# Kernel optimization log

Hardware: AMD Instinct MI355X
Metric: run time of the kernel (lower is better)

Reference implementation:

```python
import jax, jax.numpy as jnp
import numpy as np

H = 4          # attention_heads
TOPK = 101     # hard-coded [:101] in ContextModule.forward
EPS = 1e-5     # nn.LayerNorm default eps


def _linear(x, w, b):
    # torch nn.Linear: y = x @ W^T + b
    return x @ w.T + b


def _layer_norm(x, g, b):
    mu = jnp.mean(x, axis=-1, keepdims=True)
    var = jnp.var(x, axis=-1, keepdims=True)
    return (x - mu) * jax.lax.rsqrt(var + EPS) * g + b


def setup_inputs() -> dict:
    key = jax.random.key(0)
    ks = jax.random.split(key, 12)
    D, N, B, T = 512, 2000, 8, 1024
    s = 0.02
    f32 = jnp.float32
    return {
        "context_emb": jax.random.normal(ks[0], (N, D), f32),
        "encoder_out": jax.random.normal(ks[1], (B, T, D), f32),
        "wq": jax.random.normal(ks[2], (D, D), f32) * s,
        "bq": jnp.zeros((D,), f32),
        "wk": jax.random.normal(ks[3], (D, D), f32) * s,
        "bk": jnp.zeros((D,), f32),
        "wv": jax.random.normal(ks[4], (D, D), f32) * s,
        "bv": jnp.zeros((D,), f32),
        "wo": jax.random.normal(ks[5], (D, D), f32) * s,
        "bo": jnp.zeros((D,), f32),
        "w_comb": jax.random.normal(ks[6], (D, D), f32) * s,
        "b_comb": jnp.zeros((D,), f32),
        "ln_g": jnp.ones((D,), f32),
        "ln_b": jnp.zeros((D,), f32),
    }


def reference(context_emb, encoder_out, wq, bq, wk, bk, wv, bv, wo, bo,
              w_comb, b_comb, ln_g, ln_b):
    biasing_score = 1.0
    B, T, D = encoder_out.shape
    dk = D // H
    scale = 1.0 / np.sqrt(dk).astype(np.float32)

    # expand context to batch: [B, N, D]
    ctx = jnp.broadcast_to(context_emb, (B,) + context_emb.shape)

    # --- pass 1: attention matrix for scoring (get_attn_mat) ---
    q = _linear(encoder_out, wq, bq).reshape(B, T, H, dk).transpose(0, 2, 1, 3)  # bhtd
    k = _linear(ctx, wk, bk).reshape(B, -1, H, dk).transpose(0, 2, 1, 3)         # bhnd
    scores = jnp.einsum('bhtd,bhnd->bhtn', q, k) * scale
    attn = jax.nn.softmax(scores, axis=-1)                                        # [B,H,T,N]

    # attn_mat[0].sum(0).sum(0): per-context-phrase aggregate score -> [N]
    context_scores = attn[0].sum(axis=(0, 1))
    # torch.sort(descending)[1][:101] == top-101 indices by score
    _, idx = jax.lax.top_k(context_scores, TOPK)

    # gather filtered context embeddings: [B, 101, D]
    ctx_f = ctx[:, idx, :]

    # --- pass 2: full MHA on filtered context ---
    k2 = _linear(ctx_f, wk, bk).reshape(B, TOPK, H, dk).transpose(0, 2, 1, 3)
    v2 = _linear(ctx_f, wv, bv).reshape(B, TOPK, H, dk).transpose(0, 2, 1, 3)
    a2 = jax.nn.softmax(jnp.einsum('bhtd,bhnd->bhtn', q, k2) * scale, axis=-1)
    o = jnp.einsum('bhtn,bhnd->bhtd', a2, v2).transpose(0, 2, 1, 3).reshape(B, T, D)
    o = _linear(o, wo, bo)

    # combiner + residual + LayerNorm
    out = encoder_out + _linear(o, w_comb, b_comb) * biasing_score
    return _layer_norm(out, ln_g, ln_b)
```

## Files before the change

### kernel.cpp

```cpp
#include <hip/hip_runtime.h>
#include <hip/hip_bf16.h>


typedef short bhalf8 __attribute__((ext_vector_type(8)));
typedef float f32x4 __attribute__((ext_vector_type(4)));

#define SCALE 0.08838834764831845f

#define OFF_QBF    ((size_t)0)
#define OFF_RB     ((size_t)6193152)
#define OFF_TMP    ((size_t)8290304)
#define OFF_PART   (OFF_TMP)
#define OFF_CS     (OFF_TMP + 1024000)
#define OFF_IDX    (OFF_TMP + 1026048)
#define OFF_RSP    (OFF_TMP + 1026176)
#define OFF_CEBF   ((size_t)12484608)
#define OFF_K2BF   ((size_t)13022608)
#define OFF_V2TP   ((size_t)13074608)
#define OFF_WQBF   ((size_t)13107376)
#define OFF_WKBF   ((size_t)13238448)
#define OFF_WVBF   ((size_t)13369520)
#define OFF_WCBF   ((size_t)13500592)
#define OFF_WOTBF  ((size_t)13631664)
#define OFF_WC2BF  ((size_t)13762736)
#define OFF_BC2    ((size_t)13893808)

__device__ __forceinline__ float bf2f(short u) {
    union { float f; unsigned int i; } x;
    x.i = ((unsigned int)(unsigned short)u) << 16;
    return x.f;
}
__device__ __forceinline__ ushort f2b(float f) {
    union { float f; unsigned int i; } x; x.f = f;
    return (ushort)((x.i + 0x7fff + ((x.i >> 16) & 1)) >> 16);
}

__device__ __forceinline__ void gld16(ushort* lds, const ushort* g) {
    __builtin_amdgcn_global_load_lds(
        (const __attribute__((address_space(1))) unsigned int*)g,
        (__attribute__((address_space(3))) unsigned int*)lds, 16, 0, 0);
}

__global__ __launch_bounds__(256) void prep_kernel(
    const float* __restrict__ enc, const float* __restrict__ ce,
    const float* __restrict__ wq, const float* __restrict__ wk,
    const float* __restrict__ wv, const float* __restrict__ wc,
    const float* __restrict__ wo, const float* __restrict__ bo,
    const float* __restrict__ bcb,
    ushort* __restrict__ encbf, ushort* __restrict__ cebf,
    ushort* __restrict__ wqbf, ushort* __restrict__ wkbf,
    ushort* __restrict__ wvbf, ushort* __restrict__ wcbf,
    ushort* __restrict__ v2tp, ushort* __restrict__ wotbf,
    float* __restrict__ bc2)
{
    __shared__ float tile[32][33];
    const int b = blockIdx.x, tid = threadIdx.x;
    const float* s; ushort* d; int n4, base;
    if (b < 4096)      { s = enc; d = encbf; n4 = 1048576; base = b; }
    else if (b < 5096) { s = ce;  d = cebf;  n4 = 256000;  base = b - 4096; }
    else if (b < 5352) { s = wq;  d = wqbf;  n4 = 65536;   base = b - 5096; }
    else if (b < 5608) { s = wk;  d = wkbf;  n4 = 65536;   base = b - 5352; }
    else if (b < 5864) { s = wv;  d = wvbf;  n4 = 65536;   base = b - 5608; }
    else if (b < 6120) { s = wc;  d = wcbf;  n4 = 65536;   base = b - 5864; }
    else if (b < 6152) {
        const int i = (b - 6120) * 256 + tid;
        ((uint4*)v2tp)[i] = make_uint4(0u, 0u, 0u, 0u);
        return;
    } else if (b < 6154) {
        const int dd = (b - 6152) * 256 + tid;
        float acc = bcb[dd];
        const float4* wr = (const float4*)(wc + (size_t)dd * 512);
        const float4* br = (const float4*)bo;
        for (int m4 = 0; m4 < 128; ++m4) {
            const float4 w4 = wr[m4], b4 = br[m4];
            acc += w4.x * b4.x + w4.y * b4.y + w4.z * b4.z + w4.w * b4.w;
        }
        bc2[dd] = acc;
        return;
    } else {
        const int b2 = b - 6154;
        const int bx = (b2 & 15) * 32, by = (b2 >> 4) * 32;
        const int tx = tid & 31, ty = tid >> 5;
        #pragma unroll
        for (int rr = 0; rr < 4; ++rr)
            tile[ty + 8 * rr][tx] = wo[(size_t)(by + ty + 8 * rr) * 512 + bx + tx];
        __syncthreads();
        #pragma unroll
        for (int rr = 0; rr < 4; ++rr)
            wotbf[(size_t)(bx + ty + 8 * rr) * 512 + by + tx] =
                f2b(tile[tx][ty + 8 * rr]);
        return;
    }
    const int i = base * 256 + tid;
    if (i >= n4) return;
    const float4 v = ((const float4*)s)[i];
    ushort4 r;
    r.x = f2b(v.x); r.y = f2b(v.y); r.z = f2b(v.z); r.w = f2b(v.w);
    ((ushort4*)d)[i] = r;
}

__device__ __forceinline__ void gemm_body_512(
    const ushort* A, const ushort* W, const float* bias, ushort* Cbf,
    int M, int bm, int bn, ushort* As, ushort* Bs)
{
    const int tid = threadIdx.x;
    const int wave = tid >> 6, lane = tid & 63;
    const int wm = wave >> 1, wn = wave & 1;
    const int mr = lane & 15, g = lane >> 4;

    f32x4 acc[2][4];
    #pragma unroll
    for (int i = 0; i < 2; ++i)
        #pragma unroll
        for (int j = 0; j < 4; ++j)
            #pragma unroll
            for (int p = 0; p < 4; ++p) acc[i][j][p] = 0.f;

    const int r0 = tid >> 2, c0 = tid & 3;
    const int cA = (c0 ^ (r0 & 3)) * 8;
    const int rA  = min(bm + r0, M - 1);
    const ushort* gA  = A + (size_t)rA * 512 + cA;
    const ushort* gB0 = W + (size_t)(bn + r0) * 512 + cA;
    const ushort* gB1 = W + (size_t)(bn + r0 + 64) * 512 + cA;

    for (int k0 = 0; k0 < 512; k0 += 64) {
        gld16(As + wave * 512,        gA  + k0);
        gld16(As + 2048 + wave * 512, gA  + k0 + 32);
        gld16(Bs + wave * 512,        gB0 + k0);
        gld16(Bs + 4096 + wave * 512, gB0 + k0 + 32);
        gld16(Bs + 2048 + wave * 512, gB1 + k0);
        gld16(Bs + 6144 + wave * 512, gB1 + k0 + 32);
        __syncthreads();
        const int ksw = (g ^ (mr & 3)) << 3;
        #pragma unroll
        for (int h = 0; h < 2; ++h) {
            bhalf8 a[2], b[4];
            #pragma unroll
            for (int i = 0; i < 2; ++i)
                a[i] = *(const bhalf8*)
                    &As[h * 2048 + (wm * 32 + i * 16 + mr) * 32 + ksw];
            #pragma unroll
            for (int j = 0; j < 4; ++j)
                b[j] = *(const bhalf8*)
                    &Bs[h * 4096 + (wn * 64 + j * 16 + mr) * 32 + ksw];
            #pragma unroll
            for (int i = 0; i < 2; ++i)
                #pragma unroll
                for (int j = 0; j < 4; ++j)
                    acc[i][j] = __builtin_amdgcn_mfma_f32_16x16x32_bf16(
                        a[i], b[j], acc[i][j], 0, 0, 0);
        }
        __syncthreads();
    }

    #pragma unroll
    for (int i = 0; i < 2; ++i) {
        #pragma unroll
        for (int j = 0; j < 4; ++j) {
            const int gn = bn + wn * 64 + j * 16 + mr;
            const float bb = bias ? bias[gn] : 0.f;
            #pragma unroll
            for (int p = 0; p < 4; ++p) {
                const int gm = bm + wm * 32 + i * 16 + g * 4 + p;
                if (gm >= M) continue;
                Cbf[(size_t)gm * 512 + gn] = f2b(acc[i][j][p] + bb);
            }
        }
    }
}

__global__ __launch_bounds__(256) void qkc_gemm(
    const ushort* __restrict__ encbf, const ushort* __restrict__ cebf,
    const ushort* __restrict__ wcbf,
    const ushort* __restrict__ wqbf, const ushort* __restrict__ wkbf,
    const ushort* __restrict__ wotbf,
    const float* __restrict__ bq, const float* __restrict__ bk,
    ushort* __restrict__ qbf, ushort* __restrict__ kcbf,
    ushort* __restrict__ wc2bf)
{
    __shared__ __align__(16) ushort As[64 * 64];
    __shared__ __align__(16) ushort Bs[128 * 64];
    const int z = blockIdx.z;
    if (z == 1 && blockIdx.y >= 32) return;
    if (z == 2 && blockIdx.y >= 8) return;
    const ushort* A = (z == 0) ? encbf : (z == 1) ? cebf : wcbf;
    const ushort* W = (z == 0) ? wqbf : (z == 1) ? wkbf : wotbf;
    const float* bias = (z == 0) ? bq : (z == 1) ? bk : nullptr;
    ushort* C = (z == 0) ? qbf : (z == 1) ? kcbf : wc2bf;
    const int M = (z == 0) ? 8192 : (z == 1) ? 2000 : 512;
    gemm_body_512(A, W, bias, C, M, blockIdx.y * 64, blockIdx.x * 128, As, Bs);
}

__device__ __forceinline__ void stage_ktile(
    ushort* Ks, const ushort* kcbf, int nt, int h, int w, int lane)
{
    #pragma unroll
    for (int it = 0; it < 8; ++it) {
        const int u = it * 256 + (w << 6) + lane;
        const int nl = u >> 4, c = u & 15;
        gld16(Ks + (size_t)(it * 256 + (w << 6)) * 8,
              kcbf + (size_t)(nt * 128 + nl) * 512 + (h << 7)
                   + ((c ^ (nl & 7)) << 3));
    }
}

__device__ __forceinline__ void score_tile(
    const ushort* Ks, const bhalf8* aq, int mr, int g, f32x4* sacc)
{
    #pragma unroll
    for (int jn = 0; jn < 8; ++jn)
        #pragma unroll
        for (int p = 0; p < 4; ++p) sacc[jn][p] = 0.f;
    #pragma unroll
    for (int kd = 0; kd < 4; ++kd) {
        #pragma unroll
        for (int jn = 0; jn < 8; ++jn) {
            const int n = (jn << 4) + mr;
            const bhalf8 bk = *(const bhalf8*)
                &Ks[(n << 7) + ((((kd << 2) + g) ^ (n & 7)) << 3)];
            sacc[jn] = __builtin_amdgcn_mfma_f32_16x16x32_bf16(
                aq[kd], bk, sacc[jn], 0, 0, 0);
        }
    }
}

__global__ __launch_bounds__(256) void rowsum_part(
    const ushort* __restrict__ qb, const ushort* __restrict__ kcbf,
    float* __restrict__ rsp)
{
    __shared__ __align__(16) ushort Ks[128 * 128];
    const int tid = threadIdx.x, w = tid >> 6, lane = tid & 63;
    const int mr = lane & 15, g = lane >> 4;
    const int h = blockIdx.y, nc = blockIdx.z;
    const int bm = blockIdx.x * 64;

    const ushort* qrow = qb + (size_t)(bm + (w << 4) + mr) * 512 + (h << 7);
    bhalf8 aq[4];
    #pragma unroll
    for (int kd = 0; kd < 4; ++kd)
        aq[kd] = *(const bhalf8*)(qrow + (g << 3) + (kd << 5));

    float rsl[4] = {0.f, 0.f, 0.f, 0.f};
    for (int t = 0; t < 4; ++t) {
        const int nt = nc * 4 + t;
        __syncthreads();
        stage_ktile(Ks, kcbf, nt, h, w, lane);
        __syncthreads();
        f32x4 sacc[8];
        score_tile(Ks, aq, mr, g, sacc);
        #pragma unroll
        for (int jn = 0; jn < 8; ++jn) {
            const bool valid = nt * 128 + (jn << 4) + mr < 2000;
            #pragma unroll
            for (int p = 0; p < 4; ++p)
                rsl[p] += valid ? __expf(sacc[jn][p] * SCALE) : 0.f;
        }
    }
    #pragma unroll
    for (int off = 1; off <= 8; off <<= 1)
        #pragma unroll
        for (int p = 0; p < 4; ++p)
            rsl[p] += __shfl_xor(rsl[p], off);
    if (mr == 0) {
        #pragma unroll
        for (int p = 0; p < 4; ++p) {
            const int row = (h << 10) + bm + (w << 4) + (g << 2) + p;
            rsp[(size_t)row * 4 + nc] = rsl[p];
        }
    }
}

__global__ __launch_bounds__(256) void colsum_part(
    const ushort* __restrict__ qb, const ushort* __restrict__ kcbf,
    const float* __restrict__ rsp, float* __restrict__ part)
{
    __shared__ __align__(16) ushort Ks[128 * 128];
    const int tid = threadIdx.x, w = tid >> 6, lane = tid & 63;
    const int mr = lane & 15, g = lane >> 4;
    const int h = blockIdx.y, nc = blockIdx.z;
    const int bm = blockIdx.x * 64;
    const int slot = ((h * 16 + blockIdx.x) << 2) + w;

    const ushort* qrow = qb + (size_t)(bm + (w << 4) + mr) * 512 + (h << 7);
    bhalf8 aq[4];
    #pragma unroll
    for (int kd = 0; kd < 4; ++kd)
        aq[kd] = *(const bhalf8*)(qrow + (g << 3) + (kd << 5));

    float inv[4];
    #pragma unroll
    for (int p = 0; p < 4; ++p) {
        const int row = (h << 10) + bm + (w << 4) + (g << 2) + p;
        const float4 r4 = *(const float4*)(rsp + (size_t)row * 4);
        inv[p] = 1.f / (r4.x + r4.y + r4.z + r4.w);
    }

    for (int t = 0; t < 4; ++t) {
        const int nt = nc * 4 + t;
        __syncthreads();
        stage_ktile(Ks, kcbf, nt, h, w, lane);
        __syncthreads();
        f32x4 sacc[8];
        score_tile(Ks, aq, mr, g, sacc);
        #pragma unroll
        for (int jn = 0; jn < 8; ++jn) {
            const int n = nt * 128 + (jn << 4) + mr;
            const bool valid = n < 2000;
            float cv = 0.f;
            #pragma unroll
            for (int p = 0; p < 4; ++p)
                cv += valid ? __expf(sacc[jn][p] * SCALE) * inv[p] : 0.f;
            cv += __shfl_xor(cv, 16);
            cv += __shfl_xor(cv, 32);
            if (g == 0 && valid) part[(size_t)slot * 2000 + n] = cv;
        }
    }
}

__global__ __launch_bounds__(256) void reduce_full_kernel(
    const float* __restrict__ part, float* __restrict__ cs)
{
    const int n = blockIdx.x * 256 + threadIdx.x;
    if (n >= 2000) return;
    float s = 0.f;
    for (int sl = 0; sl < 256; ++sl) s += part[(size_t)sl * 2000 + n];
    cs[n] = s;
}

__global__ void topk_kernel(const float* __restrict__ cs,
                            int* __restrict__ idx)
{
    const int lane = threadIdx.x;
    const unsigned long long below = (1ull << lane) - 1ull;

    unsigned key[32];
    #pragma unroll
    for (int i = 0; i < 32; ++i) {
        const int n = lane + 64 * i;
        const float s = (n < 2000) ? cs[n] : -1e30f;
        const unsigned u = __float_as_uint(s);
        key[i] = u ^ ((unsigned)((int)u >> 31) | 0x80000000u);
    }

    unsigned prefix = 0;
    int remaining = 101;
    for (int b = 31; b >= 0; --b) {
        const unsigned tgt = (prefix << 1) | 1u;
        int cnt = 0;
        #pragma unroll
        for (int i = 0; i < 32; ++i)
            cnt += (int)__popcll(__ballot((key[i] >> b) == tgt));
        if (cnt >= remaining) prefix = tgt;
        else { remaining -= cnt; prefix = prefix << 1; }
    }
    const unsigned T = prefix;

    int base = 0;
    #pragma unroll
    for (int i = 0; i < 32; ++i) {
        const unsigned long long m = __ballot(key[i] > T);
        if (key[i] > T) idx[base + (int)__popcll(m & below)] = lane + 64 * i;
        base += (int)__popcll(m);
    }
    int r = remaining;
    #pragma unroll
    for (int i = 0; i < 32; ++i) {
        const unsigned long long m = __ballot(key[i] == T);
        const int cb = (int)__popcll(m & below);
        if (key[i] == T && cb < r) idx[base + cb] = lane + 64 * i;
        const int take = min(r, (int)__popcll(m));
        base += take; r -= take;
    }
}

__global__ __launch_bounds__(256) void kv2_proj(
    const ushort* __restrict__ cebf, const int* __restrict__ idxbuf,
    const ushort* __restrict__ wkbf, const ushort* __restrict__ wvbf,
    const float* __restrict__ bk, const float* __restrict__ bv,
    ushort* __restrict__ k2bf, ushort* __restrict__ v2tp)
{
    __shared__ __align__(16) ushort As[64 * 64];
    __shared__ __align__(16) ushort Bs[128 * 64];
    const int z = blockIdx.z;
    const ushort* W = z ? wvbf : wkbf;
    const float* bias = z ? bv : bk;
    const int tid = threadIdx.x;
    const int wave = tid >> 6, lane = tid & 63;
    const int wm = wave >> 1, wn = wave & 1;
    const int mr = lane & 15, g = lane >> 4;
    const int bm = blockIdx.y * 64, bn = blockIdx.x * 128;

    f32x4 acc[2][4];
    #pragma unroll
    for (int i = 0; i < 2; ++i)
        #pragma unroll
        for (int j = 0; j < 4; ++j)
            #pragma unroll
            for (int p = 0; p < 4; ++p) acc[i][j][p] = 0.f;

    const int r0 = tid >> 2, c0 = tid & 3;
    const int cA = (c0 ^ (r0 & 3)) * 8;
    const int rA  = min(bm + r0, 100);
    const int srcrow = idxbuf[rA];
    const ushort* gA  = cebf + (size_t)srcrow * 512 + cA;
    const ushort* gB0 = W + (size_t)(bn + r0) * 512 + cA;
    const ushort* gB1 = W + (size_t)(bn + r0 + 64) * 512 + cA;

    for (int k0 = 0; k0 < 512; k0 += 64) {
        gld16(As + wave * 512,        gA  + k0);
        gld16(As + 2048 + wave * 512, gA  + k0 + 32);
        gld16(Bs + wave * 512,        gB0 + k0);
        gld16(Bs + 4096 + wave * 512, gB0 + k0 + 32);
        gld16(Bs + 2048 + wave * 512, gB1 + k0);
        gld16(Bs + 6144 + wave * 512, gB1 + k0 + 32);
        __syncthreads();
        const int ksw = (g ^ (mr & 3)) << 3;
        #pragma unroll
        for (int h = 0; h < 2; ++h) {
            bhalf8 a[2], b[4];
            #pragma unroll
            for (int i = 0; i < 2; ++i)
                a[i] = *(const bhalf8*)
                    &As[h * 2048 + (wm * 32 + i * 16 + mr) * 32 + ksw];
            #pragma unroll
            for (int j = 0; j < 4; ++j)
                b[j] = *(const bhalf8*)
                    &Bs[h * 4096 + (wn * 64 + j * 16 + mr) * 32 + ksw];
            #pragma unroll
            for (int i = 0; i < 2; ++i)
                #pragma unroll
                for (int j = 0; j < 4; ++j)
                    acc[i][j] = __builtin_amdgcn_mfma_f32_16x16x32_bf16(
                        a[i], b[j], acc[i][j], 0, 0, 0);
        }
        __syncthreads();
    }

    #pragma unroll
    for (int i = 0; i < 2; ++i) {
        #pragma unroll
        for (int j = 0; j < 4; ++j) {
            const int gn = bn + wn * 64 + j * 16 + mr;
            const float bb = bias[gn];
            #pragma unroll
            for (int p = 0; p < 4; ++p) {
                const int gm = bm + wm * 32 + i * 16 + g * 4 + p;
                if (gm >= 101) continue;
                const ushort v = f2b(acc[i][j][p] + bb);
                if (z == 0) k2bf[(size_t)gm * 512 + gn] = v;
                else        v2tp[(size_t)gn * 128 + gm] = v;
            }
        }
    }
}

__global__ __launch_bounds__(256) void attn2_fused(
    const ushort* __restrict__ qb, const ushort* __restrict__ k2bf,
    const ushort* __restrict__ v2tp, ushort* __restrict__ obf)
{
    __shared__ __align__(16) ushort K2s[128 * 128];
    __shared__ __align__(16) ushort V2s[128 * 128];
    __shared__ __align__(16) ushort Ps[4 * 16 * 128];
    const int tid = threadIdx.x, w = tid >> 6, lane = tid & 63;
    const int mr = lane & 15, g = lane >> 4;
    const int h = blockIdx.y;
    const int bm = blockIdx.x * 64;

    #pragma unroll
    for (int it = 0; it < 8; ++it) {
        const int cl = tid + 256 * it;
        const int n = cl >> 4, c = cl & 15;
        uint4 kv = make_uint4(0u, 0u, 0u, 0u);
        if (n < 101)
            kv = *(const uint4*)(k2bf + (size_t)n * 512 + h * 128 + c * 8);
        *(uint4*)&K2s[(n << 7) + ((c ^ (n & 7)) << 3)] = kv;
        const uint4 vv = *(const uint4*)(v2tp + (((size_t)h << 7) + n) * 128 + c * 8);
        *(uint4*)&V2s[(n << 7) + ((c ^ (n & 7)) << 3)] = vv;
    }
    __syncthreads();

    f32x4 sacc[8];
    #pragma unroll
    for (int jn = 0; jn < 8; ++jn)
        #pragma unroll
        for (int p = 0; p < 4; ++p) sacc[jn][p] = 0.f;
    const ushort* qrow = qb + (size_t)(bm + (w << 4) + mr) * 512 + (h << 7);
    #pragma unroll
    for (int kd = 0; kd < 4; ++kd) {
        const bhalf8 aq = *(const bhalf8*)(qrow + (g << 3) + (kd << 5));
        #pragma unroll
        for (int jn = 0; jn < 8; ++jn) {
            const int n = (jn << 4) + mr;
            const bhalf8 bk = *(const bhalf8*)
                &K2s[(n << 7) + ((((kd << 2) + g) ^ (n & 7)) << 3)];
            sacc[jn] = __builtin_amdgcn_mfma_f32_16x16x32_bf16(aq, bk, sacc[jn], 0, 0, 0);
        }
    }

    float mrow[4] = {-1e30f, -1e30f, -1e30f, -1e30f};
    #pragma unroll
    for (int jn = 0; jn < 8; ++jn) {
        const bool valid = (jn < 6) || (jn == 6 && mr < 5);
        #pragma unroll
        for (int p = 0; p < 4; ++p) {
            const float s = valid ? sacc[jn][p] * SCALE : -1e30f;
            sacc[jn][p] = s;
            mrow[p] = fmaxf(mrow[p], s);
        }
    }
    #pragma unroll
    for (int off = 1; off <= 8; off <<= 1)
        #pragma unroll
        for (int p = 0; p < 4; ++p)
            mrow[p] = fmaxf(mrow[p], __shfl_xor(mrow[p], off));
    float srow[4] = {0.f, 0.f, 0.f, 0.f};
    #pragma unroll
    for (int jn = 0; jn < 8; ++jn)
        #pragma unroll
        for (int p = 0; p < 4; ++p) {
            const float e = __expf(sacc[jn][p] - mrow[p]);
            sacc[jn][p] = e;
            srow[p] += e;
        }
    #pragma unroll
    for (int off = 1; off <= 8; off <<= 1)
        #pragma unroll
        for (int p = 0; p < 4; ++p)
            srow[p] += __shfl_xor(srow[p], off);
    float inv[4];
    #pragma unroll
    for (int p = 0; p < 4; ++p) inv[p] = 1.f / srow[p];

    ushort* pw = Ps + (w << 11);
    #pragma unroll
    for (int jn = 0; jn < 8; ++jn) {
        const int cb = (jn << 1) + (mr >> 3);
        #pragma unroll
        for (int p = 0; p < 4; ++p) {
            const int r = (g << 2) + p;
            pw[(r << 7) + ((cb ^ (r & 7)) << 3) + (mr & 7)] =
                f2b(sacc[jn][p] * inv[p]);
        }
    }

    f32x4 oacc[8];
    #pragma unroll
    for (int jd = 0; jd < 8; ++jd)
        #pragma unroll
        for (int p = 0; p < 4; ++p) oacc[jd][p] = 0.f;
    #pragma unroll
    for (int kn = 0; kn < 4; ++kn) {
        const int ck = (kn << 2) + g;
        const bhalf8 ap = *(const bhalf8*)
            &pw[(mr << 7) + ((ck ^ (mr & 7)) << 3)];
        #pragma unroll
        for (int jd = 0; jd < 8; ++jd) {
            const int d = (jd << 4) + mr;
            const bhalf8 bv = *(const bhalf8*)
                &V2s[(d << 7) + ((ck ^ (d & 7)) << 3)];
            oacc[jd] = __builtin_amdgcn_mfma_f32_16x16x32_bf16(ap, bv, oacc[jd], 0, 0, 0);
        }
    }

    #pragma unroll
    for (int jd = 0; jd < 8; ++jd)
        #pragma unroll
        for (int p = 0; p < 4; ++p) {
            const int row = bm + (w << 4) + (g << 2) + p;
            obf[(size_t)row * 512 + (h << 7) + (jd << 4) + mr] = f2b(oacc[jd][p]);
        }
}

__global__ __launch_bounds__(256) void proj_ln(
    const ushort* __restrict__ obf, const ushort* __restrict__ wc2bf,
    const float* __restrict__ bc2, const float* __restrict__ enc,
    const float* __restrict__ gw, const float* __restrict__ bta,
    float* __restrict__ out)
{
    __shared__ __align__(16) ushort As[2 * 32 * 32];
    __shared__ __align__(16) ushort Bs[2 * 512 * 32];
    __shared__ float red1[2][32], red2[2][32];
    const int tid = threadIdx.x, w = tid >> 6, lane = tid & 63;
    const int mr = lane & 15, gq = lane >> 4;
    const int rh = w & 1, ch = w >> 1;
    const int bm = blockIdx.x * 32;

    f32x4 acc[16];
    #pragma unroll
    for (int j = 0; j < 16; ++j)
        #pragma unroll
        for (int p = 0; p < 4; ++p) acc[j][p] = 0.f;

    const int lr = lane >> 2, lc = lane & 3;
    const int swc = (lc ^ (lr & 3)) * 8;
    const ushort* gA = obf + (size_t)(bm + ((w & 1) << 4) + lr) * 512 + swc;

    for (int k0 = 0; k0 < 512; k0 += 64) {
        if (w < 2) {
            gld16(As + w * 512,        gA + k0);
            gld16(As + 1024 + w * 512, gA + k0 + 32);
        }
        #pragma unroll
        for (int r = 0; r < 8; ++r) {
            const int nb = r * 4 + w;
            const ushort* gB = wc2bf + (size_t)(nb * 16 + lr) * 512 + swc + k0;
            gld16(Bs + nb * 512,         gB);
            gld16(Bs + 16384 + nb * 512, gB + 32);
        }
        __syncthreads();
        const int ksw = (gq ^ (mr & 3)) << 3;
        #pragma unroll
        for (int h = 0; h < 2; ++h) {
            const bhalf8 a = *(const bhalf8*)
                &As[h * 1024 + (((rh << 4) + mr) << 5) + ksw];
            #pragma unroll
            for (int j = 0; j < 16; ++j) {
                const int n = (ch << 8) + (j << 4) + mr;
                const bhalf8 b = *(const bhalf8*)
                    &Bs[h * 16384 + (n << 5) + ksw];
                acc[j] = __builtin_amdgcn_mfma_f32_16x16x32_bf16(a, b, acc[j], 0, 0, 0);
            }
        }
        __syncthreads();
    }

    float s1[4] = {0.f, 0.f, 0.f, 0.f}, s2[4] = {0.f, 0.f, 0.f, 0.f};
    #pragma unroll
    for (int j = 0; j < 16; ++j) {
        const int gcol = (ch << 8) + (j << 4) + mr;
        const float bb = bc2[gcol];
        #pragma unroll
        for (int p = 0; p < 4; ++p) {
            const int grow = bm + (rh << 4) + (gq << 2) + p;
            const float x = acc[j][p] + bb + enc[(size_t)grow * 512 + gcol];
            acc[j][p] = x;
            s1[p] += x;
            s2[p] += x * x;
        }
    }
    #pragma unroll
    for (int off = 1; off <= 8; off <<= 1)
        #pragma unroll
        for (int p = 0; p < 4; ++p) {
            s1[p] += __shfl_xor(s1[p], off);
            s2[p] += __shfl_xor(s2[p], off);
        }
    if (mr == 0) {
        #pragma unroll
        for (int p = 0; p < 4; ++p) {
            red1[ch][(rh << 4) + (gq << 2) + p] = s1[p];
            red2[ch][(rh << 4) + (gq << 2) + p] = s2[p];
        }
    }
    __syncthreads();
    float mu[4], rstd[4];
    #pragma unroll
    for (int p = 0; p < 4; ++p) {
        const int ri = (rh << 4) + (gq << 2) + p;
        const float t1 = red1[0][ri] + red1[1][ri];
        const float t2 = red2[0][ri] + red2[1][ri];
        const float m = t1 * (1.f / 512.f);
        mu[p] = m;
        rstd[p] = rsqrtf(t2 * (1.f / 512.f) - m * m + 1e-5f);
    }
    #pragma unroll
    for (int j = 0; j < 16; ++j) {
        const int gcol = (ch << 8) + (j << 4) + mr;
        const float gg = gw[gcol], bb = bta[gcol];
        #pragma unroll
        for (int p = 0; p < 4; ++p) {
            const int grow = bm + (rh << 4) + (gq << 2) + p;
            out[(size_t)grow * 512 + gcol] = (acc[j][p] - mu[p]) * rstd[p] * gg + bb;
        }
    }
}

extern "C" void kernel_launch(void* const* d_in, const int* in_sizes, int n_in,
                              void* d_out, int out_size, void* d_ws, size_t ws_size,
                              hipStream_t stream)
{
    const float* ce  = (const float*)d_in[0];
    const float* enc = (const float*)d_in[1];
    const float* wq  = (const float*)d_in[2];
    const float* bq  = (const float*)d_in[3];
    const float* wk  = (const float*)d_in[4];
    const float* bk  = (const float*)d_in[5];
    const float* wv  = (const float*)d_in[6];
    const float* bv  = (const float*)d_in[7];
    const float* wo  = (const float*)d_in[8];
    const float* bo  = (const float*)d_in[9];
    const float* wc  = (const float*)d_in[10];
    const float* bcb = (const float*)d_in[11];
    const float* lng = (const float*)d_in[12];
    const float* lnb = (const float*)d_in[13];
    float* ws  = (float*)d_ws;
    float* out = (float*)d_out;

    ushort* qbf    = (ushort*)(ws + OFF_QBF);
    ushort* encbf  = (ushort*)(ws + OFF_RB);
    ushort* kcbf   = (ushort*)(ws + OFF_RB);
    ushort* obf    = (ushort*)(ws + OFF_RB);
    float*  part   = ws + OFF_PART;
    float*  cs     = ws + OFF_CS;
    int*    idx    = (int*)(ws + OFF_IDX);
    float*  rsp    = ws + OFF_RSP;
    ushort* cebf   = (ushort*)(ws + OFF_CEBF);
    ushort* k2bf   = (ushort*)(ws + OFF_K2BF);
    ushort* v2tp   = (ushort*)(ws + OFF_V2TP);
    ushort* wqbf   = (ushort*)(ws + OFF_WQBF);
    ushort* wkbf   = (ushort*)(ws + OFF_WKBF);
    ushort* wvbf   = (ushort*)(ws + OFF_WVBF);
    ushort* wcbf   = (ushort*)(ws + OFF_WCBF);
    ushort* wotbf  = (ushort*)(ws + OFF_WOTBF);
    ushort* wc2bf  = (ushort*)(ws + OFF_WC2BF);
    float*  bc2    = ws + OFF_BC2;

    prep_kernel<<<6410, 256, 0, stream>>>(enc, ce, wq, wk, wv, wc, wo, bo, bcb,
                                          encbf, cebf, wqbf, wkbf, wvbf, wcbf,
                                          v2tp, wotbf, bc2);
    qkc_gemm<<<dim3(4, 128, 3), 256, 0, stream>>>(encbf, cebf, wcbf,
                                                  wqbf, wkbf, wotbf,
                                                  bq, bk, qbf, kcbf, wc2bf);
    rowsum_part<<<dim3(16, 4, 4), 256, 0, stream>>>(qbf, kcbf, rsp);
    colsum_part<<<dim3(16, 4, 4), 256, 0, stream>>>(qbf, kcbf, rsp, part);
    reduce_full_kernel<<<8, 256, 0, stream>>>(part, cs);
    topk_kernel<<<1, 64, 0, stream>>>(cs, idx);
    kv2_proj<<<dim3(4, 2, 2), 256, 0, stream>>>(cebf, idx, wkbf, wvbf, bk, bv,
                                                k2bf, v2tp);
    attn2_fused<<<dim3(128, 4), 256, 0, stream>>>(qbf, k2bf, v2tp, obf);
    proj_ln<<<256, 256, 0, stream>>>(obf, wc2bf, bc2, enc, lng, lnb, out);
    (void)in_sizes; (void)n_in; (void)out_size; (void)ws_size;
}
```

Measured before the change: 145.9 us.

## Double-buffer GEMM smem tiles, split score passes finer, enlarge attention blocks

Adds two-stage shared-memory double buffering to the projection GEMMs so the next K-slice load is issued before computing the current one, removing one barrier per iteration. Rowsum/colsum kernels now process two key tiles per block across eight chunks, prefetching both tiles up front, doubling grid parallelism. The filtered attention kernel uses 512-thread blocks covering 128 rows. Shared memory per block grows, which may reduce occupancy, and partial-sum layout changes must match downstream reduction.

```diff
diff --git a/kernel.cpp b/kernel.cpp
--- a/kernel.cpp
+++ b/kernel.cpp
@@ -99,9 +99,21 @@
     ((ushort4*)d)[i] = r;
 }
 
+__device__ __forceinline__ void stage_ab(
+    const ushort* gA, const ushort* gB0, const ushort* gB1, int k0,
+    ushort* As, ushort* Bs, int wave)
+{
+    gld16(As + wave * 512,        gA  + k0);
+    gld16(As + 2048 + wave * 512, gA  + k0 + 32);
+    gld16(Bs + wave * 512,        gB0 + k0);
+    gld16(Bs + 4096 + wave * 512, gB0 + k0 + 32);
+    gld16(Bs + 2048 + wave * 512, gB1 + k0);
+    gld16(Bs + 6144 + wave * 512, gB1 + k0 + 32);
+}
+
 __device__ __forceinline__ void gemm_body_512(
     const ushort* A, const ushort* W, const float* bias, ushort* Cbf,
-    int M, int bm, int bn, ushort* As, ushort* Bs)
+    int M, int bm, int bn, ushort* As, ushort* Bs, int rowA)
 {
     const int tid = threadIdx.x;
     const int wave = tid >> 6, lane = tid & 63;
@@ -118,19 +130,19 @@
 
     const int r0 = tid >> 2, c0 = tid & 3;
     const int cA = (c0 ^ (r0 & 3)) * 8;
-    const int rA  = min(bm + r0, M - 1);
-    const ushort* gA  = A + (size_t)rA * 512 + cA;
+    const ushort* gA  = A + (size_t)rowA * 512 + cA;
     const ushort* gB0 = W + (size_t)(bn + r0) * 512 + cA;
     const ushort* gB1 = W + (size_t)(bn + r0 + 64) * 512 + cA;
 
+    stage_ab(gA, gB0, gB1, 0, As, Bs, wave);
     for (int k0 = 0; k0 < 512; k0 += 64) {
-        gld16(As + wave * 512,        gA  + k0);
-        gld16(As + 2048 + wave * 512, gA  + k0 + 32);
-        gld16(Bs + wave * 512,        gB0 + k0);
-        gld16(Bs + 4096 + wave * 512, gB0 + k0 + 32);
-        gld16(Bs + 2048 + wave * 512, gB1 + k0);
-        gld16(Bs + 6144 + wave * 512, gB1 + k0 + 32);
+        const int cur = (k0 >> 6) & 1;
+        ushort* Ac = As + cur * 4096;
+        ushort* Bc = Bs + cur * 8192;
         __syncthreads();
+        if (k0 + 64 < 512)
+            stage_ab(gA, gB0, gB1, k0 + 64,
+                     As + (cur ^ 1) * 4096, Bs + (cur ^ 1) * 8192, wave);
         const int ksw = (g ^ (mr & 3)) << 3;
         #pragma unroll
         for (int h = 0; h < 2; ++h) {
@@ -138,11 +150,11 @@
             #pragma unroll
             for (int i = 0; i < 2; ++i)
                 a[i] = *(const bhalf8*)
-                    &As[h * 2048 + (wm * 32 + i * 16 + mr) * 32 + ksw];
+                    &Ac[h * 2048 + (wm * 32 + i * 16 + mr) * 32 + ksw];
             #pragma unroll
             for (int j = 0; j < 4; ++j)
                 b[j] = *(const bhalf8*)
-                    &Bs[h * 4096 + (wn * 64 + j * 16 + mr) * 32 + ksw];
+                    &Bc[h * 4096 + (wn * 64 + j * 16 + mr) * 32 + ksw];
             #pragma unroll
             for (int i = 0; i < 2; ++i)
                 #pragma unroll
@@ -150,7 +162,6 @@
                     acc[i][j] = __builtin_amdgcn_mfma_f32_16x16x32_bf16(
                         a[i], b[j], acc[i][j], 0, 0, 0);
         }
-        __syncthreads();
     }
 
     #pragma unroll
@@ -178,8 +189,8 @@
     ushort* __restrict__ qbf, ushort* __restrict__ kcbf,
     ushort* __restrict__ wc2bf)
 {
-    __shared__ __align__(16) ushort As[64 * 64];
-    __shared__ __align__(16) ushort Bs[128 * 64];
+    __shared__ __align__(16) ushort As[2 * 64 * 64];
+    __shared__ __align__(16) ushort Bs[2 * 128 * 64];
     const int z = blockIdx.z;
     if (z == 1 && blockIdx.y >= 32) return;
     if (z == 2 && blockIdx.y >= 8) return;
@@ -188,7 +199,9 @@
     const float* bias = (z == 0) ? bq : (z == 1) ? bk : nullptr;
     ushort* C = (z == 0) ? qbf : (z == 1) ? kcbf : wc2bf;
     const int M = (z == 0) ? 8192 : (z == 1) ? 2000 : 512;
-    gemm_body_512(A, W, bias, C, M, blockIdx.y * 64, blockIdx.x * 128, As, Bs);
+    const int bm = blockIdx.y * 64;
+    const int rowA = min(bm + (threadIdx.x >> 2), M - 1);
+    gemm_body_512(A, W, bias, C, M, bm, blockIdx.x * 128, As, Bs, rowA);
 }
 
 __device__ __forceinline__ void stage_ktile(
@@ -228,7 +241,7 @@
     const ushort* __restrict__ qb, const ushort* __restrict__ kcbf,
     float* __restrict__ rsp)
 {
-    __shared__ __align__(16) ushort Ks[128 * 128];
+    __shared__ __align__(16) ushort Ks[2 * 128 * 128];
     const int tid = threadIdx.x, w = tid >> 6, lane = tid & 63;
     const int mr = lane & 15, g = lane >> 4;
     const int h = blockIdx.y, nc = blockIdx.z;
@@ -240,22 +253,31 @@
     for (int kd = 0; kd < 4; ++kd)
         aq[kd] = *(const bhalf8*)(qrow + (g << 3) + (kd << 5));
 
+    const int nt0 = nc * 2, nt1 = nc * 2 + 1;
+    stage_ktile(Ks, kcbf, nt0, h, w, lane);
+    __syncthreads();
+    stage_ktile(Ks + 16384, kcbf, nt1, h, w, lane);
+
     float rsl[4] = {0.f, 0.f, 0.f, 0.f};
-    for (int t = 0; t < 4; ++t) {
-        const int nt = nc * 4 + t;
-        __syncthreads();
-        stage_ktile(Ks, kcbf, nt, h, w, lane);
-        __syncthreads();
-        f32x4 sacc[8];
-        score_tile(Ks, aq, mr, g, sacc);
-        #pragma unroll
-        for (int jn = 0; jn < 8; ++jn) {
-            const bool valid = nt * 128 + (jn << 4) + mr < 2000;
-            #pragma unroll
-            for (int p = 0; p < 4; ++p)
-                rsl[p] += valid ? __expf(sacc[jn][p] * SCALE) : 0.f;
-        }
-    }
+    f32x4 sacc[8];
+    score_tile(Ks, aq, mr, g, sacc);
+    #pragma unroll
+    for (int jn = 0; jn < 8; ++jn) {
+        const bool valid = nt0 * 128 + (jn << 4) + mr < 2000;
+        #pragma unroll
+        for (int p = 0; p < 4; ++p)
+            rsl[p] += valid ? __expf(sacc[jn][p] * SCALE) : 0.f;
+    }
+    __syncthreads();
+    score_tile(Ks + 16384, aq, mr, g, sacc);
+    #pragma unroll
+    for (int jn = 0; jn < 8; ++jn) {
+        const bool valid = nt1 * 128 + (jn << 4) + mr < 2000;
+        #pragma unroll
+        for (int p = 0; p < 4; ++p)
+            rsl[p] += valid ? __expf(sacc[jn][p] * SCALE) : 0.f;
+    }
+
     #pragma unroll
     for (int off = 1; off <= 8; off <<= 1)
         #pragma unroll
@@ -265,7 +287,7 @@
         #pragma unroll
         for (int p = 0; p < 4; ++p) {
             const int row = (h << 10) + bm + (w << 4) + (g << 2) + p;
-            rsp[(size_t)row * 4 + nc] = rsl[p];
+            rsp[(size_t)row * 8 + nc] = rsl[p];
         }
     }
 }
@@ -274,7 +296,7 @@
     const ushort* __restrict__ qb, const ushort* __restrict__ kcbf,
     const float* __restrict__ rsp, float* __restrict__ part)
 {
-    __shared__ __align__(16) ushort Ks[128 * 128];
+    __shared__ __align__(16) ushort Ks[2 * 128 * 128];
     const int tid = threadIdx.x, w = tid >> 6, lane = tid & 63;
     const int mr = lane & 15, g = lane >> 4;
     const int h = blockIdx.y, nc = blockIdx.z;
@@ -291,17 +313,22 @@
     #pragma unroll
     for (int p = 0; p < 4; ++p) {
         const int row = (h << 10) + bm + (w << 4) + (g << 2) + p;
-        const float4 r4 = *(const float4*)(rsp + (size_t)row * 4);
-        inv[p] = 1.f / (r4.x + r4.y + r4.z + r4.w);
-    }
-
-    for (int t = 0; t < 4; ++t) {
-        const int nt = nc * 4 + t;
-        __syncthreads();
-        stage_ktile(Ks, kcbf, nt, h, w, lane);
-        __syncthreads();
-        f32x4 sacc[8];
-        score_tile(Ks, aq, mr, g, sacc);
+        const float4 ra = *(const float4*)(rsp + (size_t)row * 8);
+        const float4 rb = *(const float4*)(rsp + (size_t)row * 8 + 4);
+        inv[p] = 1.f / (ra.x + ra.y + ra.z + ra.w + rb.x + rb.y + rb.z + rb.w);
+    }
+
+    const int nt0 = nc * 2, nt1 = nc * 2 + 1;
+    stage_ktile(Ks, kcbf, nt0, h, w, lane);
+    __syncthreads();
+    stage_ktile(Ks + 16384, kcbf, nt1, h, w, lane);
+
+    f32x4 sacc[8];
+    #pragma unroll
+    for (int t = 0; t < 2; ++t) {
+        if (t == 1) __syncthreads();
+        const int nt = t ? nt1 : nt0;
+        score_tile(t ? Ks + 16384 : Ks, aq, mr, g, sacc);
         #pragma unroll
         for (int jn = 0; jn < 8; ++jn) {
             const int n = nt * 128 + (jn << 4) + mr;
@@ -379,8 +406,8 @@
     const float* __restrict__ bk, const float* __restrict__ bv,
     ushort* __restrict__ k2bf, ushort* __restrict__ v2tp)
 {
-    __shared__ __align__(16) ushort As[64 * 64];
-    __shared__ __align__(16) ushort Bs[128 * 64];
+    __shared__ __align__(16) ushort As[2 * 64 * 64];
+    __shared__ __align__(16) ushort Bs[2 * 128 * 64];
     const int z = blockIdx.z;
     const ushort* W = z ? wvbf : wkbf;
     const float* bias = z ? bv : bk;
@@ -406,14 +433,15 @@
     const ushort* gB0 = W + (size_t)(bn + r0) * 512 + cA;
     const ushort* gB1 = W + (size_t)(bn + r0 + 64) * 512 + cA;
 
+    stage_ab(gA, gB0, gB1, 0, As, Bs, wave);
     for (int k0 = 0; k0 < 512; k0 += 64) {
-        gld16(As + wave * 512,        gA  + k0);
-        gld16(As + 2048 + wave * 512, gA  + k0 + 32);
-        gld16(Bs + wave * 512,        gB0 + k0);
-        gld16(Bs + 4096 + wave * 512, gB0 + k0 + 32);
-        gld16(Bs + 2048 + wave * 512, gB1 + k0);
-        gld16(Bs + 6144 + wave * 512, gB1 + k0 + 32);
+        const int cur = (k0 >> 6) & 1;
+        ushort* Ac = As + cur * 4096;
+        ushort* Bc = Bs + cur * 8192;
         __syncthreads();
+        if (k0 + 64 < 512)
+            stage_ab(gA, gB0, gB1, k0 + 64,
+                     As + (cur ^ 1) * 4096, Bs + (cur ^ 1) * 8192, wave);
         const int ksw = (g ^ (mr & 3)) << 3;
         #pragma unroll
         for (int h = 0; h < 2; ++h) {
@@ -421,11 +449,11 @@
             #pragma unroll
             for (int i = 0; i < 2; ++i)
                 a[i] = *(const bhalf8*)
-                    &As[h * 2048 + (wm * 32 + i * 16 + mr) * 32 + ksw];
+                    &Ac[h * 2048 + (wm * 32 + i * 16 + mr) * 32 + ksw];
             #pragma unroll
             for (int j = 0; j < 4; ++j)
                 b[j] = *(const bhalf8*)
-                    &Bs[h * 4096 + (wn * 64 + j * 16 + mr) * 32 + ksw];
+                    &Bc[h * 4096 + (wn * 64 + j * 16 + mr) * 32 + ksw];
             #pragma unroll
             for (int i = 0; i < 2; ++i)
                 #pragma unroll
@@ -433,7 +461,6 @@
                     acc[i][j] = __builtin_amdgcn_mfma_f32_16x16x32_bf16(
                         a[i], b[j], acc[i][j], 0, 0, 0);
         }
-        __syncthreads();
     }
 
     #pragma unroll
@@ -454,21 +481,21 @@
     }
 }
 
-__global__ __launch_bounds__(256) void attn2_fused(
+__global__ __launch_bounds__(512) void attn2_fused(
     const ushort* __restrict__ qb, const ushort* __restrict__ k2bf,
     const ushort* __restrict__ v2tp, ushort* __restrict__ obf)
 {
     __shared__ __align__(16) ushort K2s[128 * 128];
     __shared__ __align__(16) ushort V2s[128 * 128];
-    __shared__ __align__(16) ushort Ps[4 * 16 * 128];
+    __shared__ __align__(16) ushort Ps[8 * 16 * 128];
     const int tid = threadIdx.x, w = tid >> 6, lane = tid & 63;
     const int mr = lane & 15, g = lane >> 4;
     const int h = blockIdx.y;
-    const int bm = blockIdx.x * 64;
-
-    #pragma unroll
-    for (int it = 0; it < 8; ++it) {
-        const int cl = tid + 256 * it;
+    const int bm = blockIdx.x * 128;
+
+    #pragma unroll
+    for (int it = 0; it < 4; ++it) {
+        const int cl = tid + 512 * it;
         const int n = cl >> 4, c = cl & 15;
         uint4 kv = make_uint4(0u, 0u, 0u, 0u);
         if (n < 101)
@@ -571,14 +598,30 @@
         }
 }
 
+__device__ __forceinline__ void pl_stage(
+    const ushort* gA, const ushort* gB, int k0,
+    ushort* Asb, ushort* Bsb, int w)
+{
+    if (w < 2) {
+        gld16(Asb + w * 512,        gA + k0);
+        gld16(Asb + 1024 + w * 512, gA + k0 + 32);
+    }
+    #pragma unroll
+    for (int r = 0; r < 8; ++r) {
+        const int nb = r * 4 + w;
+        gld16(Bsb + nb * 512,         gB + nb * 8192 + k0);
+        gld16(Bsb + 16384 + nb * 512, gB + nb * 8192 + k0 + 32);
+    }
+}
+
 __global__ __launch_bounds__(256) void proj_ln(
     const ushort* __restrict__ obf, const ushort* __restrict__ wc2bf,
     const float* __restrict__ bc2, const float* __restrict__ enc,
     const float* __restrict__ gw, const float* __restrict__ bta,
     float* __restrict__ out)
 {
-    __shared__ __align__(16) ushort As[2 * 32 * 32];
-    __shared__ __align__(16) ushort Bs[2 * 512 * 32];
+    __shared__ __align__(16) ushort As[2 * 2048];
+    __shared__ __align__(16) ushort Bs[2 * 32768];
     __shared__ float red1[2][32], red2[2][32];
     const int tid = threadIdx.x, w = tid >> 6, lane = tid & 63;
     const int mr = lane & 15, gq = lane >> 4;
@@ -594,34 +637,30 @@
     const int lr = lane >> 2, lc = lane & 3;
     const int swc = (lc ^ (lr & 3)) * 8;
     const ushort* gA = obf + (size_t)(bm + ((w & 1) << 4) + lr) * 512 + swc;
-
+    const ushort* gB = wc2bf + (size_t)lr * 512 + swc;
+
+    pl_stage(gA, gB, 0, As, Bs, w);
     for (int k0 = 0; k0 < 512; k0 += 64) {
-        if (w < 2) {
-            gld16(As + w * 512,        gA + k0);
-            gld16(As + 1024 + w * 512, gA + k0 + 32);
-        }
-        #pragma unroll
-        for (int r = 0; r < 8; ++r) {
-            const int nb = r * 4 + w;
-            const ushort* gB = wc2bf + (size_t)(nb * 16 + lr) * 512 + swc + k0;
-            gld16(Bs + nb * 512,         gB);
-            gld16(Bs + 16384 + nb * 512, gB + 32);
-        }
+        const int cur = (k0 >> 6) & 1;
+        ushort* Ac = As + cur * 2048;
+        ushort* Bc = Bs + cur * 32768;
         __syncthreads();
+        if (k0 + 64 < 512)
+            pl_stage(gA, gB, k0 + 64,
+                     As + (cur ^ 1) * 2048, Bs + (cur ^ 1) * 32768, w);
         const int ksw = (gq ^ (mr & 3)) << 3;
         #pragma unroll
         for (int h = 0; h < 2; ++h) {
             const bhalf8 a = *(const bhalf8*)
-                &As[h * 1024 + (((rh << 4) + mr) << 5) + ksw];
+                &Ac[h * 1024 + (((rh << 4) + mr) << 5) + ksw];
             #pragma unroll
             for (int j = 0; j < 16; ++j) {
                 const int n = (ch << 8) + (j << 4) + mr;
                 const bhalf8 b = *(const bhalf8*)
-                    &Bs[h * 16384 + (n << 5) + ksw];
+                    &Bc[h * 16384 + (n << 5) + ksw];
                 acc[j] = __builtin_amdgcn_mfma_f32_16x16x32_bf16(a, b, acc[j], 0, 0, 0);
             }
         }
-        __syncthreads();
     }
 
     float s1[4] = {0.f, 0.f, 0.f, 0.f}, s2[4] = {0.f, 0.f, 0.f, 0.f};
@@ -721,13 +760,13 @@
     qkc_gemm<<<dim3(4, 128, 3), 256, 0, stream>>>(encbf, cebf, wcbf,
                                                   wqbf, wkbf, wotbf,
                                                   bq, bk, qbf, kcbf, wc2bf);
-    rowsum_part<<<dim3(16, 4, 4), 256, 0, stream>>>(qbf, kcbf, rsp);
-    colsum_part<<<dim3(16, 4, 4), 256, 0, stream>>>(qbf, kcbf, rsp, part);
+    rowsum_part<<<dim3(16, 4, 8), 256, 0, stream>>>(qbf, kcbf, rsp);
+    colsum_part<<<dim3(16, 4, 8), 256, 0, stream>>>(qbf, kcbf, rsp, part);
     reduce_full_kernel<<<8, 256, 0, stream>>>(part, cs);
     topk_kernel<<<1, 64, 0, stream>>>(cs, idx);
     kv2_proj<<<dim3(4, 2, 2), 256, 0, stream>>>(cebf, idx, wkbf, wvbf, bk, bv,
                                                 k2bf, v2tp);
-    attn2_fused<<<dim3(128, 4), 256, 0, stream>>>(qbf, k2bf, v2tp, obf);
+    attn2_fused<<<dim3(64, 4), 512, 0, stream>>>(qbf, k2bf, v2tp, obf);
     proj_ln<<<256, 256, 0, stream>>>(obf, wc2bf, bc2, enc, lng, lnb, out);
     (void)in_sizes; (void)n_in; (void)out_size; (void)ws_size;
 }
```

Result: faster. 136.0 us (-6.8%).
